# Performance work log

Measured on AMD Instinct MI355X. Metric: run time of the kernel, lower is better.

Reference implementation:

```python
import jax, jax.numpy as jnp
import numpy as np

N = 50000          # nodes
E = 600000         # edges
D = 128            # g_dim = h1_dim = h2_dim
R = 8              # 2 * n_speakers**2, n_speakers=2
B = 10             # num_bases


def setup_inputs() -> dict:
    key = jax.random.key(0)
    ks = jax.random.split(key, 10)
    s = 1.0 / np.sqrt(D)
    return {
        "node_features": jax.random.normal(ks[0], (N, D), jnp.float32),
        "edge_index": jax.random.randint(ks[1], (2, E), 0, N, jnp.int64),
        "edge_type": jax.random.randint(ks[2], (E,), 0, R, jnp.int64),
        # RGCNConv params (basis decomposition)
        "basis": jax.random.normal(ks[3], (B, D, D), jnp.float32) * s,
        "comp": jax.random.normal(ks[4], (R, B), jnp.float32) * (1.0 / np.sqrt(B)),
        "root": jax.random.normal(ks[5], (D, D), jnp.float32) * s,
        "bias1": jnp.zeros((D,), jnp.float32),
        # GraphConv params
        "w_rel": jax.random.normal(ks[6], (D, D), jnp.float32) * s,
        "b_rel": jnp.zeros((D,), jnp.float32),
        "w_root": jax.random.normal(ks[7], (D, D), jnp.float32) * s,
    }


def reference(node_features, edge_index, edge_type, basis, comp, root, bias1, w_rel, b_rel, w_root):
    x = node_features
    n = x.shape[0]
    r = comp.shape[0]
    src, dst = edge_index[0], edge_index[1]

    # ---- RGCNConv (basis decomposition, per-relation mean aggregation) ----
    # project through bases once: [N, B, D]
    xb = jnp.einsum('ni,bio->nbo', x, basis)
    # per-edge message: combine bases with relation coefficients  [E, D]
    msg = jnp.einsum('eb,ebo->eo', comp[edge_type], xb[src])
    # per-(dst, relation) mean normalization
    seg = dst * r + edge_type                       # [E]
    cnt = jax.ops.segment_sum(jnp.ones((msg.shape[0],), x.dtype), seg, num_segments=n * r)
    norm = 1.0 / jnp.maximum(cnt[seg], 1.0)         # [E]
    agg = jax.ops.segment_sum(msg * norm[:, None], dst, num_segments=n)  # [N, D]
    h1 = agg + x @ root + bias1

    # ---- GraphConv (add aggregation of neighbors + root transform) ----
    nbr = jax.ops.segment_sum(h1[src], dst, num_segments=n)  # [N, D]
    out = nbr @ w_rel.T + b_rel + h1 @ w_root.T
    return out
```

## Files before the change

### kernel.cpp

```cpp
#include <hip/hip_runtime.h>
#include <stdint.h>

#define N_NODES 50000
#define E_EDGES 600000
#define D 128
#define R_REL 8
#define B_BASES 10
#define RN (R_REL * N_NODES)
#define SCAN_B 1024

typedef __attribute__((ext_vector_type(8))) short bf16x8;
typedef __attribute__((ext_vector_type(4))) float f32x4;

__device__ __forceinline__ short f2b(float f) {
    uint32_t u = __float_as_uint(f);
    u += 0x7fff + ((u >> 16) & 1);
    return (short)(u >> 16);
}
__device__ __forceinline__ float b2f(uint16_t u) {
    return __uint_as_float((uint32_t)u << 16);
}

__global__ __launch_bounds__(256) void k_prep(const float* __restrict__ basis,
                                              const float* __restrict__ comp,
                                              const float* __restrict__ root,
                                              const float* __restrict__ wrel,
                                              const float* __restrict__ wroot,
                                              short* __restrict__ wt,
                                              short* __restrict__ root_t,
                                              short* __restrict__ wrel_b,
                                              short* __restrict__ wroot_b) {
    int tid = blockIdx.x * 256 + threadIdx.x;
    if (tid < R_REL * D * D) {
        int r = tid >> 14;
        int rem = tid & 16383;
        int j = rem >> 7, i = rem & 127;
        float s = 0.f;
#pragma unroll
        for (int b = 0; b < B_BASES; b++)
            s += comp[r * B_BASES + b] * basis[b * D * D + i * D + j];
        wt[tid] = f2b(s);
    } else {
        int t2 = tid - R_REL * D * D;
        if (t2 < D * D) {
            int j = t2 >> 7, i = t2 & 127;
            root_t[t2]  = f2b(root[i * D + j]);
            wrel_b[t2]  = f2b(wrel[t2]);
            wroot_b[t2] = f2b(wroot[t2]);
        }
    }
}

__global__ __launch_bounds__(256) void k_x2b(const float* __restrict__ x,
                                             unsigned short* __restrict__ xb) {
    int tid = blockIdx.x * 256 + threadIdx.x;
    if (tid >= N_NODES * D / 8) return;
    const float4* s = (const float4*)x + (size_t)tid * 2;
    float4 v0 = s[0], v1 = s[1];
    union { uint4 u; unsigned short h[8]; } pk;
    pk.h[0] = (unsigned short)f2b(v0.x); pk.h[1] = (unsigned short)f2b(v0.y);
    pk.h[2] = (unsigned short)f2b(v0.z); pk.h[3] = (unsigned short)f2b(v0.w);
    pk.h[4] = (unsigned short)f2b(v1.x); pk.h[5] = (unsigned short)f2b(v1.y);
    pk.h[6] = (unsigned short)f2b(v1.z); pk.h[7] = (unsigned short)f2b(v1.w);
    ((uint4*)xb)[tid] = pk.u;
}

__global__ __launch_bounds__(256) void k_count(const int* __restrict__ dst,
                                               const int* __restrict__ et,
                                               int* __restrict__ cntr) {
    int e = blockIdx.x * 256 + threadIdx.x;
    if (e >= E_EDGES) return;
    atomicAdd(&cntr[dst[e] * R_REL + et[e]], 1);
}

__global__ __launch_bounds__(SCAN_B) void k_scan_a(const int* __restrict__ in,
                                                   int* __restrict__ out,
                                                   int* __restrict__ bsum, int n) {
    __shared__ int lds[SCAN_B];
    int t = threadIdx.x, g = blockIdx.x * SCAN_B + t;
    int v = (g < n) ? in[g] : 0;
    lds[t] = v;
    __syncthreads();
    for (int off = 1; off < SCAN_B; off <<= 1) {
        int tv = (t >= off) ? lds[t - off] : 0;
        __syncthreads();
        lds[t] += tv;
        __syncthreads();
    }
    if (g < n) out[g] = lds[t] - v;
    if (t == SCAN_B - 1) bsum[blockIdx.x] = lds[t];
}

__global__ __launch_bounds__(SCAN_B) void k_scan_b(int* __restrict__ bsum, int nb) {
    __shared__ int lds[SCAN_B];
    int t = threadIdx.x;
    int v = (t < nb) ? bsum[t] : 0;
    lds[t] = v;
    __syncthreads();
    for (int off = 1; off < SCAN_B; off <<= 1) {
        int tv = (t >= off) ? lds[t - off] : 0;
        __syncthreads();
        lds[t] += tv;
        __syncthreads();
    }
    if (t < nb) bsum[t] = lds[t] - v;
}

__global__ __launch_bounds__(SCAN_B) void k_scan_c(int* __restrict__ out,
                                                   const int* __restrict__ bsum, int n) {
    int g = blockIdx.x * SCAN_B + threadIdx.x;
    if (g < n) out[g] += bsum[blockIdx.x];
}

__global__ __launch_bounds__(256) void k_bucket(const int* __restrict__ src,
                                                const int* __restrict__ dst,
                                                const int* __restrict__ et,
                                                const int* __restrict__ seg_off,
                                                int* __restrict__ cur,
                                                int* __restrict__ es1) {
    int e = blockIdx.x * 256 + threadIdx.x;
    if (e >= E_EDGES) return;
    int key = dst[e] * R_REL + et[e];
    int pos = seg_off[key] + atomicAdd(&cur[key], 1);
    es1[pos] = src[e];
}

__global__ __launch_bounds__(256) void k_ygemm(const unsigned short* __restrict__ xb,
                                               const short* __restrict__ wt, int r0,
                                               unsigned short* __restrict__ ybig) {
    __shared__ short xs[64 * 128];
    __shared__ short ws[128 * 128];
    int slice = blockIdx.y;
    const short* w = wt + (size_t)(r0 + slice) * D * D;
    unsigned short* y = ybig + (size_t)slice * N_NODES * D;
    int base = blockIdx.x * 64;
    int t = threadIdx.x;
    const uint4* wsrc = (const uint4*)w;
    for (int idx = t; idx < 2048; idx += 256) {
        int j = idx >> 4, c = idx & 15;
        *(uint4*)&ws[j * 128 + ((c ^ (j & 15)) << 3)] = wsrc[idx];
    }
    for (int idx = t; idx < 1024; idx += 256) {
        int row = idx >> 4, c = idx & 15;
        int node = base + row;
        uint4 v = make_uint4(0, 0, 0, 0);
        if (node < N_NODES) v = ((const uint4*)(xb + (size_t)node * D))[c];
        *(uint4*)&xs[row * 128 + ((c ^ (row & 15)) << 3)] = v;
    }
    __syncthreads();

    int wave = t >> 6, lane = t & 63, quad = lane >> 4, l16 = lane & 15;
    f32x4 acc[8];
#pragma unroll
    for (int jt = 0; jt < 8; jt++) acc[jt] = (f32x4){0.f, 0.f, 0.f, 0.f};
#pragma unroll
    for (int kc = 0; kc < 4; kc++) {
        int c0 = kc * 4 + quad;
        bf16x8 a = *(const bf16x8*)&xs[(wave * 16 + l16) * 128 + ((c0 ^ l16) << 3)];
#pragma unroll
        for (int jt = 0; jt < 8; jt++) {
            bf16x8 b = *(const bf16x8*)&ws[(jt * 16 + l16) * 128 + ((c0 ^ l16) << 3)];
            acc[jt] = __builtin_amdgcn_mfma_f32_16x16x32_bf16(a, b, acc[jt], 0, 0, 0);
        }
    }
#pragma unroll
    for (int reg = 0; reg < 4; reg++) {
        int node = base + wave * 16 + quad * 4 + reg;
        if (node >= N_NODES) continue;
#pragma unroll
        for (int jt = 0; jt < 8; jt++)
            y[(size_t)node * D + jt * 16 + l16] = (unsigned short)f2b(acc[jt][reg]);
    }
}

__global__ __launch_bounds__(256) void k_gemm_root(const unsigned short* __restrict__ inb,
                                                   const short* __restrict__ bt,
                                                   const float* __restrict__ bias,
                                                   const float* __restrict__ prev,
                                                   unsigned short* __restrict__ outb) {
    __shared__ short xs[64 * 128];
    __shared__ short ws[128 * 128];
    int base = blockIdx.x * 64;
    int t = threadIdx.x;
    const uint4* wsrc = (const uint4*)bt;
    for (int idx = t; idx < 2048; idx += 256) {
        int j = idx >> 4, c = idx & 15;
        *(uint4*)&ws[j * 128 + ((c ^ (j & 15)) << 3)] = wsrc[idx];
    }
    for (int idx = t; idx < 1024; idx += 256) {
        int row = idx >> 4, c = idx & 15;
        int node = base + row;
        uint4 v = make_uint4(0, 0, 0, 0);
        if (node < N_NODES) v = ((const uint4*)(inb + (size_t)node * D))[c];
        *(uint4*)&xs[row * 128 + ((c ^ (row & 15)) << 3)] = v;
    }
    __syncthreads();

    int wave = t >> 6, lane = t & 63, quad = lane >> 4, l16 = lane & 15;
    f32x4 acc[8];
#pragma unroll
    for (int jt = 0; jt < 8; jt++) acc[jt] = (f32x4){0.f, 0.f, 0.f, 0.f};
#pragma unroll
    for (int kc = 0; kc < 4; kc++) {
        int c0 = kc * 4 + quad;
        bf16x8 a = *(const bf16x8*)&xs[(wave * 16 + l16) * 128 + ((c0 ^ l16) << 3)];
#pragma unroll
        for (int jt = 0; jt < 8; jt++) {
            bf16x8 b = *(const bf16x8*)&ws[(jt * 16 + l16) * 128 + ((c0 ^ l16) << 3)];
            acc[jt] = __builtin_amdgcn_mfma_f32_16x16x32_bf16(a, b, acc[jt], 0, 0, 0);
        }
    }
#pragma unroll
    for (int reg = 0; reg < 4; reg++) {
        int node = base + wave * 16 + quad * 4 + reg;
        if (node >= N_NODES) continue;
#pragma unroll
        for (int jt = 0; jt < 8; jt++) {
            int col = jt * 16 + l16;
            float v = acc[jt][reg] + bias[col] + prev[(size_t)node * D + col];
            outb[(size_t)node * D + col] = (unsigned short)f2b(v);
        }
    }
}

__global__ __launch_bounds__(256) void k_agg4(const unsigned short* __restrict__ y,
                                              const int* __restrict__ es1,
                                              const int* __restrict__ cntr,
                                              const int* __restrict__ seg_off,
                                              float* __restrict__ h1, int phase) {
    int t = threadIdx.x;
    int wave = t >> 6, lane = t & 63, sub = lane >> 4, l = lane & 15;
    int d = blockIdx.x * 16 + wave * 4 + sub;
    if (d >= N_NODES) return;
    int kb = d * R_REL + phase * 4;
    int b0 = seg_off[kb], b1 = seg_off[kb + 1], b2 = seg_off[kb + 2], b3 = seg_off[kb + 3];
    int c3 = cntr[kb + 3];
    int end = b3 + c3;
    int c0 = b1 - b0, c1 = b2 - b1, c2 = b3 - b2;
    float n0 = c0 ? 1.f / (float)c0 : 0.f;
    float n1 = c1 ? 1.f / (float)c1 : 0.f;
    float n2 = c2 ? 1.f / (float)c2 : 0.f;
    float n3 = c3 ? 1.f / (float)c3 : 0.f;

    float acc[8];
#pragma unroll
    for (int j = 0; j < 8; j++) acc[j] = 0.f;
    size_t loff = (size_t)l * 8;

    int pos = b0;
    for (; pos + 4 <= end; pos += 4) {
        int i0 = es1[pos], i1 = es1[pos + 1], i2 = es1[pos + 2], i3 = es1[pos + 3];
        float m0 = (pos     >= b1) ? ((pos     >= b3) ? n3 : (pos     >= b2) ? n2 : n1) : n0;
        float m1 = (pos + 1 >= b1) ? ((pos + 1 >= b3) ? n3 : (pos + 1 >= b2) ? n2 : n1) : n0;
        float m2 = (pos + 2 >= b1) ? ((pos + 2 >= b3) ? n3 : (pos + 2 >= b2) ? n2 : n1) : n0;
        float m3 = (pos + 3 >= b1) ? ((pos + 3 >= b3) ? n3 : (pos + 3 >= b2) ? n2 : n1) : n0;
        int r0 = (pos     >= b1) + (pos     >= b2) + (pos     >= b3);
        int r1 = (pos + 1 >= b1) + (pos + 1 >= b2) + (pos + 1 >= b3);
        int r2 = (pos + 2 >= b1) + (pos + 2 >= b2) + (pos + 2 >= b3);
        int r3 = (pos + 3 >= b1) + (pos + 3 >= b2) + (pos + 3 >= b3);
        uint4 v0 = *(const uint4*)(y + ((size_t)r0 * N_NODES + i0) * D + loff);
        uint4 v1 = *(const uint4*)(y + ((size_t)r1 * N_NODES + i1) * D + loff);
        uint4 v2 = *(const uint4*)(y + ((size_t)r2 * N_NODES + i2) * D + loff);
        uint4 v3 = *(const uint4*)(y + ((size_t)r3 * N_NODES + i3) * D + loff);
        const uint32_t* w0 = (const uint32_t*)&v0;
        const uint32_t* w1 = (const uint32_t*)&v1;
        const uint32_t* w2 = (const uint32_t*)&v2;
        const uint32_t* w3 = (const uint32_t*)&v3;
#pragma unroll
        for (int q = 0; q < 4; q++) {
            acc[q * 2]     += m0 * b2f((uint16_t)w0[q]) + m1 * b2f((uint16_t)w1[q]) +
                              m2 * b2f((uint16_t)w2[q]) + m3 * b2f((uint16_t)w3[q]);
            acc[q * 2 + 1] += m0 * b2f((uint16_t)(w0[q] >> 16)) + m1 * b2f((uint16_t)(w1[q] >> 16)) +
                              m2 * b2f((uint16_t)(w2[q] >> 16)) + m3 * b2f((uint16_t)(w3[q] >> 16));
        }
    }
    for (; pos < end; pos++) {
        int i0 = es1[pos];
        float m0 = (pos >= b1) ? ((pos >= b3) ? n3 : (pos >= b2) ? n2 : n1) : n0;
        int r0 = (pos >= b1) + (pos >= b2) + (pos >= b3);
        uint4 v0 = *(const uint4*)(y + ((size_t)r0 * N_NODES + i0) * D + loff);
        const uint32_t* w0 = (const uint32_t*)&v0;
#pragma unroll
        for (int q = 0; q < 4; q++) {
            acc[q * 2]     += m0 * b2f((uint16_t)w0[q]);
            acc[q * 2 + 1] += m0 * b2f((uint16_t)(w0[q] >> 16));
        }
    }

    float* hr = h1 + (size_t)d * D + loff;
    if (phase) {
#pragma unroll
        for (int j = 0; j < 8; j++) acc[j] += hr[j];
    }
    *(float4*)hr = make_float4(acc[0], acc[1], acc[2], acc[3]);
    *(float4*)(hr + 4) = make_float4(acc[4], acc[5], acc[6], acc[7]);
}

__global__ __launch_bounds__(256) void k_agg_nbr(const unsigned short* __restrict__ h1b,
                                                 const int* __restrict__ es1,
                                                 const int* __restrict__ seg_off,
                                                 unsigned short* __restrict__ nbr) {
    int t = threadIdx.x;
    int wave = t >> 6, lane = t & 63, sub = lane >> 4, l = lane & 15;
    int d = blockIdx.x * 16 + wave * 4 + sub;
    if (d >= N_NODES) return;
    int s0 = seg_off[d * R_REL];
    int end = (d == N_NODES - 1) ? E_EDGES : seg_off[(d + 1) * R_REL];
    float acc[8];
#pragma unroll
    for (int j = 0; j < 8; j++) acc[j] = 0.f;
    size_t loff = (size_t)l * 8;

    int pos = s0;
    for (; pos + 4 <= end; pos += 4) {
        int i0 = es1[pos], i1 = es1[pos + 1], i2 = es1[pos + 2], i3 = es1[pos + 3];
        uint4 v0 = *(const uint4*)(h1b + (size_t)i0 * D + loff);
        uint4 v1 = *(const uint4*)(h1b + (size_t)i1 * D + loff);
        uint4 v2 = *(const uint4*)(h1b + (size_t)i2 * D + loff);
        uint4 v3 = *(const uint4*)(h1b + (size_t)i3 * D + loff);
        const uint32_t* w0 = (const uint32_t*)&v0;
        const uint32_t* w1 = (const uint32_t*)&v1;
        const uint32_t* w2 = (const uint32_t*)&v2;
        const uint32_t* w3 = (const uint32_t*)&v3;
#pragma unroll
        for (int q = 0; q < 4; q++) {
            acc[q * 2]     += b2f((uint16_t)w0[q]) + b2f((uint16_t)w1[q]) +
                              b2f((uint16_t)w2[q]) + b2f((uint16_t)w3[q]);
            acc[q * 2 + 1] += b2f((uint16_t)(w0[q] >> 16)) + b2f((uint16_t)(w1[q] >> 16)) +
                              b2f((uint16_t)(w2[q] >> 16)) + b2f((uint16_t)(w3[q] >> 16));
        }
    }
    for (; pos < end; pos++) {
        int i0 = es1[pos];
        uint4 v0 = *(const uint4*)(h1b + (size_t)i0 * D + loff);
        const uint32_t* w0 = (const uint32_t*)&v0;
#pragma unroll
        for (int q = 0; q < 4; q++) {
            acc[q * 2]     += b2f((uint16_t)w0[q]);
            acc[q * 2 + 1] += b2f((uint16_t)(w0[q] >> 16));
        }
    }

    union { uint4 u; unsigned short h[8]; } pk;
#pragma unroll
    for (int j = 0; j < 8; j++) pk.h[j] = (unsigned short)f2b(acc[j]);
    *(uint4*)(nbr + (size_t)d * D + loff) = pk.u;
}

__global__ __launch_bounds__(256) void k_out2(const unsigned short* __restrict__ h1b,
                                              const unsigned short* __restrict__ nbr,
                                              const short* __restrict__ wroot_b,
                                              const short* __restrict__ wrel_b,
                                              const float* __restrict__ brel,
                                              float* __restrict__ out) {
    __shared__ short xs1[64 * 128];
    __shared__ short xs2[64 * 128];
    __shared__ short ws1[128 * 128];
    __shared__ short ws2[128 * 128];
    int base = blockIdx.x * 64;
    int t = threadIdx.x;
    const uint4* w1 = (const uint4*)wroot_b;
    const uint4* w2 = (const uint4*)wrel_b;
    for (int idx = t; idx < 2048; idx += 256) {
        int j = idx >> 4, c = idx & 15;
        int sw = j * 128 + ((c ^ (j & 15)) << 3);
        *(uint4*)&ws1[sw] = w1[idx];
        *(uint4*)&ws2[sw] = w2[idx];
    }
    for (int idx = t; idx < 1024; idx += 256) {
        int row = idx >> 4, c = idx & 15;
        int node = base + row;
        uint4 v1 = make_uint4(0, 0, 0, 0), v2 = make_uint4(0, 0, 0, 0);
        if (node < N_NODES) {
            v1 = ((const uint4*)(h1b + (size_t)node * D))[c];
            v2 = ((const uint4*)(nbr + (size_t)node * D))[c];
        }
        int sw = row * 128 + ((c ^ (row & 15)) << 3);
        *(uint4*)&xs1[sw] = v1;
        *(uint4*)&xs2[sw] = v2;
    }
    __syncthreads();

    int wave = t >> 6, lane = t & 63, quad = lane >> 4, l16 = lane & 15;
    f32x4 acc[8];
#pragma unroll
    for (int jt = 0; jt < 8; jt++) acc[jt] = (f32x4){0.f, 0.f, 0.f, 0.f};
#pragma unroll
    for (int kc = 0; kc < 4; kc++) {
        int c0 = kc * 4 + quad;
        int arow = (wave * 16 + l16) * 128 + ((c0 ^ l16) << 3);
        bf16x8 a1 = *(const bf16x8*)&xs1[arow];
        bf16x8 a2 = *(const bf16x8*)&xs2[arow];
#pragma unroll
        for (int jt = 0; jt < 8; jt++) {
            int brow = (jt * 16 + l16) * 128 + ((c0 ^ l16) << 3);
            bf16x8 b1 = *(const bf16x8*)&ws1[brow];
            bf16x8 b2 = *(const bf16x8*)&ws2[brow];
            acc[jt] = __builtin_amdgcn_mfma_f32_16x16x32_bf16(a1, b1, acc[jt], 0, 0, 0);
            acc[jt] = __builtin_amdgcn_mfma_f32_16x16x32_bf16(a2, b2, acc[jt], 0, 0, 0);
        }
    }
#pragma unroll
    for (int reg = 0; reg < 4; reg++) {
        int node = base + wave * 16 + quad * 4 + reg;
        if (node >= N_NODES) continue;
#pragma unroll
        for (int jt = 0; jt < 8; jt++) {
            int col = jt * 16 + l16;
            out[(size_t)node * D + col] = acc[jt][reg] + brel[col];
        }
    }
}

extern "C" void kernel_launch(void* const* d_in, const int* in_sizes, int n_in,
                              void* d_out, int out_size, void* d_ws, size_t ws_size,
                              hipStream_t stream) {
    const float* x     = (const float*)d_in[0];
    const int*   ei    = (const int*)d_in[1];
    const int*   et    = (const int*)d_in[2];
    const float* basis = (const float*)d_in[3];
    const float* comp  = (const float*)d_in[4];
    const float* root  = (const float*)d_in[5];
    const float* bias1 = (const float*)d_in[6];
    const float* wrel  = (const float*)d_in[7];
    const float* brel  = (const float*)d_in[8];
    const float* wroot = (const float*)d_in[9];
    float* out = (float*)d_out;
    const int* src = ei;
    const int* dst = ei + E_EDGES;

    char* p = (char*)d_ws;
    auto alloc = [&](size_t bytes) { char* q = p; p += (bytes + 255) & ~(size_t)255; return q; };
    short* wt      = (short*)alloc((size_t)R_REL * D * D * sizeof(short));
    short* root_t  = (short*)alloc(D * D * sizeof(short));
    short* wrel_b  = (short*)alloc(D * D * sizeof(short));
    short* wroot_b = (short*)alloc(D * D * sizeof(short));
    int*   cntr    = (int*)alloc((size_t)2 * RN * sizeof(int));
    int*   cur     = cntr + RN;
    int*   seg_off = (int*)alloc((size_t)RN * sizeof(int));
    int*   es1     = (int*)alloc((size_t)(E_EDGES + 16) * sizeof(int));
    int*   bsum    = (int*)alloc(SCAN_B * sizeof(int));
    unsigned short* xb   = (unsigned short*)alloc((size_t)N_NODES * D * sizeof(unsigned short));
    unsigned short* ybig = (unsigned short*)alloc((size_t)4 * N_NODES * D * sizeof(unsigned short));
    float* h1      = (float*)alloc((size_t)N_NODES * D * sizeof(float));
    unsigned short* h1b  = (unsigned short*)alloc((size_t)N_NODES * D * sizeof(unsigned short));
    unsigned short* nbr  = xb;

    hipMemsetAsync(cntr, 0, (size_t)2 * RN * sizeof(int), stream);

    k_prep<<<(R_REL * D * D + D * D + 255) / 256, 256, 0, stream>>>(
        basis, comp, root, wrel, wroot, wt, root_t, wrel_b, wroot_b);
    k_x2b<<<(N_NODES * D / 8 + 255) / 256, 256, 0, stream>>>(x, xb);
    k_count<<<(E_EDGES + 255) / 256, 256, 0, stream>>>(dst, et, cntr);

    int nscan = (RN + SCAN_B - 1) / SCAN_B;
    k_scan_a<<<nscan, SCAN_B, 0, stream>>>(cntr, seg_off, bsum, RN);
    k_scan_b<<<1, SCAN_B, 0, stream>>>(bsum, nscan);
    k_scan_c<<<nscan, SCAN_B, 0, stream>>>(seg_off, bsum, RN);

    k_bucket<<<(E_EDGES + 255) / 256, 256, 0, stream>>>(src, dst, et, seg_off, cur, es1);

    int nb = (N_NODES + 63) / 64;
    int na = (N_NODES + 15) / 16;

    k_ygemm<<<dim3(nb, 4), 256, 0, stream>>>(xb, wt, 0, ybig);
    k_agg4<<<na, 256, 0, stream>>>(ybig, es1, cntr, seg_off, h1, 0);
    k_ygemm<<<dim3(nb, 4), 256, 0, stream>>>(xb, wt, 4, ybig);
    k_agg4<<<na, 256, 0, stream>>>(ybig, es1, cntr, seg_off, h1, 1);

    k_gemm_root<<<nb, 256, 0, stream>>>(xb, root_t, bias1, h1, h1b);
    k_agg_nbr<<<na, 256, 0, stream>>>(h1b, es1, seg_off, nbr);
    k_out2<<<nb, 256, 0, stream>>>(h1b, nbr, wroot_b, wrel_b, brel, out);
}
```

Measured before the change: 325.5 us.

## Merge relation GEMMs with root GEMM, single-pass aggregation, wave-shuffle scan

Folds the root transform in as a ninth weight slice, so one batched GEMM writes all nine projections and a single aggregation kernel produces h1 in bf16 without an fp32 intermediate or a second pass. The bucket step now increments seg_off in place, so seg_off ends up holding segment end offsets. It packs the relation into each edge index and precomputes per-edge norms, removing per-position branch logic. Smaller launches are merged (cast and count fused, scan uses wave shuffles, the scan-b kernel is reused), and the cur counter array is dropped. The trade-off is a larger ybig buffer (9 slices instead of 4) and an extra per-edge norm array to read.

```diff
diff --git a/kernel.cpp b/kernel.cpp
--- a/kernel.cpp
+++ b/kernel.cpp
@@ -7,7 +7,6 @@
 #define R_REL 8
 #define B_BASES 10
 #define RN (R_REL * N_NODES)
-#define SCAN_B 1024
 
 typedef __attribute__((ext_vector_type(8))) short bf16x8;
 typedef __attribute__((ext_vector_type(4))) float f32x4;
@@ -27,111 +26,113 @@
                                               const float* __restrict__ wrel,
                                               const float* __restrict__ wroot,
                                               short* __restrict__ wt,
-                                              short* __restrict__ root_t,
                                               short* __restrict__ wrel_b,
                                               short* __restrict__ wroot_b) {
     int tid = blockIdx.x * 256 + threadIdx.x;
-    if (tid < R_REL * D * D) {
-        int r = tid >> 14;
+    if (tid < 9 * D * D) {
+        int s = tid >> 14;
         int rem = tid & 16383;
         int j = rem >> 7, i = rem & 127;
-        float s = 0.f;
-#pragma unroll
-        for (int b = 0; b < B_BASES; b++)
-            s += comp[r * B_BASES + b] * basis[b * D * D + i * D + j];
-        wt[tid] = f2b(s);
+        float v;
+        if (s < 8) {
+            v = 0.f;
+#pragma unroll
+            for (int b = 0; b < B_BASES; b++)
+                v += comp[s * B_BASES + b] * basis[b * D * D + i * D + j];
+        } else {
+            v = root[i * D + j];
+        }
+        wt[tid] = f2b(v);
     } else {
-        int t2 = tid - R_REL * D * D;
+        int t2 = tid - 9 * D * D;
         if (t2 < D * D) {
-            int j = t2 >> 7, i = t2 & 127;
-            root_t[t2]  = f2b(root[i * D + j]);
             wrel_b[t2]  = f2b(wrel[t2]);
             wroot_b[t2] = f2b(wroot[t2]);
         }
     }
 }
 
-__global__ __launch_bounds__(256) void k_x2b(const float* __restrict__ x,
-                                             unsigned short* __restrict__ xb) {
+__global__ __launch_bounds__(256) void k_misc(const float* __restrict__ x,
+                                              unsigned short* __restrict__ xb,
+                                              const int* __restrict__ dst,
+                                              const int* __restrict__ et,
+                                              int* __restrict__ cntr) {
     int tid = blockIdx.x * 256 + threadIdx.x;
-    if (tid >= N_NODES * D / 8) return;
-    const float4* s = (const float4*)x + (size_t)tid * 2;
-    float4 v0 = s[0], v1 = s[1];
-    union { uint4 u; unsigned short h[8]; } pk;
-    pk.h[0] = (unsigned short)f2b(v0.x); pk.h[1] = (unsigned short)f2b(v0.y);
-    pk.h[2] = (unsigned short)f2b(v0.z); pk.h[3] = (unsigned short)f2b(v0.w);
-    pk.h[4] = (unsigned short)f2b(v1.x); pk.h[5] = (unsigned short)f2b(v1.y);
-    pk.h[6] = (unsigned short)f2b(v1.z); pk.h[7] = (unsigned short)f2b(v1.w);
-    ((uint4*)xb)[tid] = pk.u;
-}
-
-__global__ __launch_bounds__(256) void k_count(const int* __restrict__ dst,
-                                               const int* __restrict__ et,
-                                               int* __restrict__ cntr) {
-    int e = blockIdx.x * 256 + threadIdx.x;
-    if (e >= E_EDGES) return;
-    atomicAdd(&cntr[dst[e] * R_REL + et[e]], 1);
-}
-
-__global__ __launch_bounds__(SCAN_B) void k_scan_a(const int* __restrict__ in,
-                                                   int* __restrict__ out,
-                                                   int* __restrict__ bsum, int n) {
-    __shared__ int lds[SCAN_B];
-    int t = threadIdx.x, g = blockIdx.x * SCAN_B + t;
+    if (tid < N_NODES * D / 8) {
+        const float4* s = (const float4*)x + (size_t)tid * 2;
+        float4 v0 = s[0], v1 = s[1];
+        union { uint4 u; unsigned short h[8]; } pk;
+        pk.h[0] = (unsigned short)f2b(v0.x); pk.h[1] = (unsigned short)f2b(v0.y);
+        pk.h[2] = (unsigned short)f2b(v0.z); pk.h[3] = (unsigned short)f2b(v0.w);
+        pk.h[4] = (unsigned short)f2b(v1.x); pk.h[5] = (unsigned short)f2b(v1.y);
+        pk.h[6] = (unsigned short)f2b(v1.z); pk.h[7] = (unsigned short)f2b(v1.w);
+        ((uint4*)xb)[tid] = pk.u;
+    } else {
+        int e = tid - N_NODES * D / 8;
+        if (e < E_EDGES)
+            atomicAdd(&cntr[dst[e] * R_REL + et[e]], 1);
+    }
+}
+
+__device__ __forceinline__ int wave_scan_incl(int v) {
+    int lane = threadIdx.x & 63;
+#pragma unroll
+    for (int off = 1; off < 64; off <<= 1) {
+        int n = __shfl_up(v, off, 64);
+        if (lane >= off) v += n;
+    }
+    return v;
+}
+
+__global__ __launch_bounds__(1024) void k_scan_a(const int* __restrict__ in,
+                                                 int* __restrict__ out,
+                                                 int* __restrict__ bsum, int n) {
+    __shared__ int wsum[16];
+    int t = threadIdx.x, lane = t & 63, wid = t >> 6;
+    int g = blockIdx.x * 1024 + t;
     int v = (g < n) ? in[g] : 0;
-    lds[t] = v;
+    int isc = wave_scan_incl(v);
+    if (lane == 63) wsum[wid] = isc;
     __syncthreads();
-    for (int off = 1; off < SCAN_B; off <<= 1) {
-        int tv = (t >= off) ? lds[t - off] : 0;
-        __syncthreads();
-        lds[t] += tv;
-        __syncthreads();
-    }
-    if (g < n) out[g] = lds[t] - v;
-    if (t == SCAN_B - 1) bsum[blockIdx.x] = lds[t];
-}
-
-__global__ __launch_bounds__(SCAN_B) void k_scan_b(int* __restrict__ bsum, int nb) {
-    __shared__ int lds[SCAN_B];
-    int t = threadIdx.x;
-    int v = (t < nb) ? bsum[t] : 0;
-    lds[t] = v;
+    if (wid == 0) {
+        int wv = (lane < 16) ? wsum[lane] : 0;
+        int wsc = wave_scan_incl(wv);
+        if (lane < 16) wsum[lane] = wsc - wv;
+    }
     __syncthreads();
-    for (int off = 1; off < SCAN_B; off <<= 1) {
-        int tv = (t >= off) ? lds[t - off] : 0;
-        __syncthreads();
-        lds[t] += tv;
-        __syncthreads();
-    }
-    if (t < nb) bsum[t] = lds[t] - v;
-}
-
-__global__ __launch_bounds__(SCAN_B) void k_scan_c(int* __restrict__ out,
-                                                   const int* __restrict__ bsum, int n) {
-    int g = blockIdx.x * SCAN_B + threadIdx.x;
+    if (g < n) out[g] = wsum[wid] + isc - v;
+    if (t == 1023 && bsum) bsum[blockIdx.x] = wsum[15] + isc;
+}
+
+__global__ __launch_bounds__(1024) void k_scan_c(int* __restrict__ out,
+                                                 const int* __restrict__ bsum, int n) {
+    int g = blockIdx.x * 1024 + threadIdx.x;
     if (g < n) out[g] += bsum[blockIdx.x];
 }
 
 __global__ __launch_bounds__(256) void k_bucket(const int* __restrict__ src,
                                                 const int* __restrict__ dst,
                                                 const int* __restrict__ et,
-                                                const int* __restrict__ seg_off,
-                                                int* __restrict__ cur,
-                                                int* __restrict__ es1) {
+                                                const int* __restrict__ cntr,
+                                                int* __restrict__ seg_off,
+                                                int* __restrict__ es1,
+                                                float* __restrict__ enorm) {
     int e = blockIdx.x * 256 + threadIdx.x;
     if (e >= E_EDGES) return;
-    int key = dst[e] * R_REL + et[e];
-    int pos = seg_off[key] + atomicAdd(&cur[key], 1);
-    es1[pos] = src[e];
+    int r = et[e];
+    int key = dst[e] * R_REL + r;
+    int pos = atomicAdd(&seg_off[key], 1);
+    es1[pos] = (src[e] << 3) | r;
+    enorm[pos] = 1.0f / (float)cntr[key];
 }
 
 __global__ __launch_bounds__(256) void k_ygemm(const unsigned short* __restrict__ xb,
-                                               const short* __restrict__ wt, int r0,
+                                               const short* __restrict__ wt,
                                                unsigned short* __restrict__ ybig) {
     __shared__ short xs[64 * 128];
     __shared__ short ws[128 * 128];
     int slice = blockIdx.y;
-    const short* w = wt + (size_t)(r0 + slice) * D * D;
+    const short* w = wt + (size_t)slice * D * D;
     unsigned short* y = ybig + (size_t)slice * N_NODES * D;
     int base = blockIdx.x * 64;
     int t = threadIdx.x;
@@ -173,95 +174,31 @@
     }
 }
 
-__global__ __launch_bounds__(256) void k_gemm_root(const unsigned short* __restrict__ inb,
-                                                   const short* __restrict__ bt,
-                                                   const float* __restrict__ bias,
-                                                   const float* __restrict__ prev,
-                                                   unsigned short* __restrict__ outb) {
-    __shared__ short xs[64 * 128];
-    __shared__ short ws[128 * 128];
-    int base = blockIdx.x * 64;
-    int t = threadIdx.x;
-    const uint4* wsrc = (const uint4*)bt;
-    for (int idx = t; idx < 2048; idx += 256) {
-        int j = idx >> 4, c = idx & 15;
-        *(uint4*)&ws[j * 128 + ((c ^ (j & 15)) << 3)] = wsrc[idx];
-    }
-    for (int idx = t; idx < 1024; idx += 256) {
-        int row = idx >> 4, c = idx & 15;
-        int node = base + row;
-        uint4 v = make_uint4(0, 0, 0, 0);
-        if (node < N_NODES) v = ((const uint4*)(inb + (size_t)node * D))[c];
-        *(uint4*)&xs[row * 128 + ((c ^ (row & 15)) << 3)] = v;
-    }
-    __syncthreads();
-
-    int wave = t >> 6, lane = t & 63, quad = lane >> 4, l16 = lane & 15;
-    f32x4 acc[8];
-#pragma unroll
-    for (int jt = 0; jt < 8; jt++) acc[jt] = (f32x4){0.f, 0.f, 0.f, 0.f};
-#pragma unroll
-    for (int kc = 0; kc < 4; kc++) {
-        int c0 = kc * 4 + quad;
-        bf16x8 a = *(const bf16x8*)&xs[(wave * 16 + l16) * 128 + ((c0 ^ l16) << 3)];
-#pragma unroll
-        for (int jt = 0; jt < 8; jt++) {
-            bf16x8 b = *(const bf16x8*)&ws[(jt * 16 + l16) * 128 + ((c0 ^ l16) << 3)];
-            acc[jt] = __builtin_amdgcn_mfma_f32_16x16x32_bf16(a, b, acc[jt], 0, 0, 0);
-        }
-    }
-#pragma unroll
-    for (int reg = 0; reg < 4; reg++) {
-        int node = base + wave * 16 + quad * 4 + reg;
-        if (node >= N_NODES) continue;
-#pragma unroll
-        for (int jt = 0; jt < 8; jt++) {
-            int col = jt * 16 + l16;
-            float v = acc[jt][reg] + bias[col] + prev[(size_t)node * D + col];
-            outb[(size_t)node * D + col] = (unsigned short)f2b(v);
-        }
-    }
-}
-
-__global__ __launch_bounds__(256) void k_agg4(const unsigned short* __restrict__ y,
+__global__ __launch_bounds__(256) void k_agg8(const unsigned short* __restrict__ ybig,
                                               const int* __restrict__ es1,
-                                              const int* __restrict__ cntr,
+                                              const float* __restrict__ enorm,
                                               const int* __restrict__ seg_off,
-                                              float* __restrict__ h1, int phase) {
+                                              const float* __restrict__ bias1,
+                                              unsigned short* __restrict__ h1b) {
     int t = threadIdx.x;
     int wave = t >> 6, lane = t & 63, sub = lane >> 4, l = lane & 15;
     int d = blockIdx.x * 16 + wave * 4 + sub;
     if (d >= N_NODES) return;
-    int kb = d * R_REL + phase * 4;
-    int b0 = seg_off[kb], b1 = seg_off[kb + 1], b2 = seg_off[kb + 2], b3 = seg_off[kb + 3];
-    int c3 = cntr[kb + 3];
-    int end = b3 + c3;
-    int c0 = b1 - b0, c1 = b2 - b1, c2 = b3 - b2;
-    float n0 = c0 ? 1.f / (float)c0 : 0.f;
-    float n1 = c1 ? 1.f / (float)c1 : 0.f;
-    float n2 = c2 ? 1.f / (float)c2 : 0.f;
-    float n3 = c3 ? 1.f / (float)c3 : 0.f;
-
+    int start = (d == 0) ? 0 : seg_off[d * R_REL - 1];
+    int end = seg_off[d * R_REL + 7];
     float acc[8];
 #pragma unroll
     for (int j = 0; j < 8; j++) acc[j] = 0.f;
     size_t loff = (size_t)l * 8;
 
-    int pos = b0;
+    int pos = start;
     for (; pos + 4 <= end; pos += 4) {
-        int i0 = es1[pos], i1 = es1[pos + 1], i2 = es1[pos + 2], i3 = es1[pos + 3];
-        float m0 = (pos     >= b1) ? ((pos     >= b3) ? n3 : (pos     >= b2) ? n2 : n1) : n0;
-        float m1 = (pos + 1 >= b1) ? ((pos + 1 >= b3) ? n3 : (pos + 1 >= b2) ? n2 : n1) : n0;
-        float m2 = (pos + 2 >= b1) ? ((pos + 2 >= b3) ? n3 : (pos + 2 >= b2) ? n2 : n1) : n0;
-        float m3 = (pos + 3 >= b1) ? ((pos + 3 >= b3) ? n3 : (pos + 3 >= b2) ? n2 : n1) : n0;
-        int r0 = (pos     >= b1) + (pos     >= b2) + (pos     >= b3);
-        int r1 = (pos + 1 >= b1) + (pos + 1 >= b2) + (pos + 1 >= b3);
-        int r2 = (pos + 2 >= b1) + (pos + 2 >= b2) + (pos + 2 >= b3);
-        int r3 = (pos + 3 >= b1) + (pos + 3 >= b2) + (pos + 3 >= b3);
-        uint4 v0 = *(const uint4*)(y + ((size_t)r0 * N_NODES + i0) * D + loff);
-        uint4 v1 = *(const uint4*)(y + ((size_t)r1 * N_NODES + i1) * D + loff);
-        uint4 v2 = *(const uint4*)(y + ((size_t)r2 * N_NODES + i2) * D + loff);
-        uint4 v3 = *(const uint4*)(y + ((size_t)r3 * N_NODES + i3) * D + loff);
+        int p0 = es1[pos], p1 = es1[pos + 1], p2 = es1[pos + 2], p3 = es1[pos + 3];
+        float m0 = enorm[pos], m1 = enorm[pos + 1], m2 = enorm[pos + 2], m3 = enorm[pos + 3];
+        uint4 v0 = *(const uint4*)(ybig + ((size_t)(p0 & 7) * N_NODES + (p0 >> 3)) * D + loff);
+        uint4 v1 = *(const uint4*)(ybig + ((size_t)(p1 & 7) * N_NODES + (p1 >> 3)) * D + loff);
+        uint4 v2 = *(const uint4*)(ybig + ((size_t)(p2 & 7) * N_NODES + (p2 >> 3)) * D + loff);
+        uint4 v3 = *(const uint4*)(ybig + ((size_t)(p3 & 7) * N_NODES + (p3 >> 3)) * D + loff);
         const uint32_t* w0 = (const uint32_t*)&v0;
         const uint32_t* w1 = (const uint32_t*)&v1;
         const uint32_t* w2 = (const uint32_t*)&v2;
@@ -275,10 +212,9 @@
         }
     }
     for (; pos < end; pos++) {
-        int i0 = es1[pos];
-        float m0 = (pos >= b1) ? ((pos >= b3) ? n3 : (pos >= b2) ? n2 : n1) : n0;
-        int r0 = (pos >= b1) + (pos >= b2) + (pos >= b3);
-        uint4 v0 = *(const uint4*)(y + ((size_t)r0 * N_NODES + i0) * D + loff);
+        int p0 = es1[pos];
+        float m0 = enorm[pos];
+        uint4 v0 = *(const uint4*)(ybig + ((size_t)(p0 & 7) * N_NODES + (p0 >> 3)) * D + loff);
         const uint32_t* w0 = (const uint32_t*)&v0;
 #pragma unroll
         for (int q = 0; q < 4; q++) {
@@ -287,13 +223,18 @@
         }
     }
 
-    float* hr = h1 + (size_t)d * D + loff;
-    if (phase) {
-#pragma unroll
-        for (int j = 0; j < 8; j++) acc[j] += hr[j];
-    }
-    *(float4*)hr = make_float4(acc[0], acc[1], acc[2], acc[3]);
-    *(float4*)(hr + 4) = make_float4(acc[4], acc[5], acc[6], acc[7]);
+    uint4 rv = *(const uint4*)(ybig + ((size_t)8 * N_NODES + d) * D + loff);
+    const uint32_t* rw = (const uint32_t*)&rv;
+    float4 ba = *(const float4*)(bias1 + l * 8);
+    float4 bb = *(const float4*)(bias1 + l * 8 + 4);
+    float bv[8] = {ba.x, ba.y, ba.z, ba.w, bb.x, bb.y, bb.z, bb.w};
+    union { uint4 u; unsigned short h[8]; } pk;
+#pragma unroll
+    for (int q = 0; q < 4; q++) {
+        pk.h[q * 2]     = (unsigned short)f2b(acc[q * 2] + b2f((uint16_t)rw[q]) + bv[q * 2]);
+        pk.h[q * 2 + 1] = (unsigned short)f2b(acc[q * 2 + 1] + b2f((uint16_t)(rw[q] >> 16)) + bv[q * 2 + 1]);
+    }
+    *(uint4*)(h1b + (size_t)d * D + loff) = pk.u;
 }
 
 __global__ __launch_bounds__(256) void k_agg_nbr(const unsigned short* __restrict__ h1b,
@@ -304,16 +245,17 @@
     int wave = t >> 6, lane = t & 63, sub = lane >> 4, l = lane & 15;
     int d = blockIdx.x * 16 + wave * 4 + sub;
     if (d >= N_NODES) return;
-    int s0 = seg_off[d * R_REL];
-    int end = (d == N_NODES - 1) ? E_EDGES : seg_off[(d + 1) * R_REL];
+    int start = (d == 0) ? 0 : seg_off[d * R_REL - 1];
+    int end = seg_off[d * R_REL + 7];
     float acc[8];
 #pragma unroll
     for (int j = 0; j < 8; j++) acc[j] = 0.f;
     size_t loff = (size_t)l * 8;
 
-    int pos = s0;
+    int pos = start;
     for (; pos + 4 <= end; pos += 4) {
-        int i0 = es1[pos], i1 = es1[pos + 1], i2 = es1[pos + 2], i3 = es1[pos + 3];
+        int i0 = es1[pos] >> 3, i1 = es1[pos + 1] >> 3;
+        int i2 = es1[pos + 2] >> 3, i3 = es1[pos + 3] >> 3;
         uint4 v0 = *(const uint4*)(h1b + (size_t)i0 * D + loff);
         uint4 v1 = *(const uint4*)(h1b + (size_t)i1 * D + loff);
         uint4 v2 = *(const uint4*)(h1b + (size_t)i2 * D + loff);
@@ -331,7 +273,7 @@
         }
     }
     for (; pos < end; pos++) {
-        int i0 = es1[pos];
+        int i0 = es1[pos] >> 3;
         uint4 v0 = *(const uint4*)(h1b + (size_t)i0 * D + loff);
         const uint32_t* w0 = (const uint32_t*)&v0;
 #pragma unroll
@@ -431,44 +373,37 @@
 
     char* p = (char*)d_ws;
     auto alloc = [&](size_t bytes) { char* q = p; p += (bytes + 255) & ~(size_t)255; return q; };
-    short* wt      = (short*)alloc((size_t)R_REL * D * D * sizeof(short));
-    short* root_t  = (short*)alloc(D * D * sizeof(short));
+    short* wt      = (short*)alloc((size_t)9 * D * D * sizeof(short));
     short* wrel_b  = (short*)alloc(D * D * sizeof(short));
     short* wroot_b = (short*)alloc(D * D * sizeof(short));
-    int*   cntr    = (int*)alloc((size_t)2 * RN * sizeof(int));
-    int*   cur     = cntr + RN;
+    int*   cntr    = (int*)alloc((size_t)RN * sizeof(int));
     int*   seg_off = (int*)alloc((size_t)RN * sizeof(int));
     int*   es1     = (int*)alloc((size_t)(E_EDGES + 16) * sizeof(int));
-    int*   bsum    = (int*)alloc(SCAN_B * sizeof(int));
+    float* enorm   = (float*)alloc((size_t)(E_EDGES + 16) * sizeof(float));
+    int*   bsum    = (int*)alloc(1024 * sizeof(int));
     unsigned short* xb   = (unsigned short*)alloc((size_t)N_NODES * D * sizeof(unsigned short));
-    unsigned short* ybig = (unsigned short*)alloc((size_t)4 * N_NODES * D * sizeof(unsigned short));
-    float* h1      = (float*)alloc((size_t)N_NODES * D * sizeof(float));
+    unsigned short* ybig = (unsigned short*)alloc((size_t)9 * N_NODES * D * sizeof(unsigned short));
     unsigned short* h1b  = (unsigned short*)alloc((size_t)N_NODES * D * sizeof(unsigned short));
     unsigned short* nbr  = xb;
 
-    hipMemsetAsync(cntr, 0, (size_t)2 * RN * sizeof(int), stream);
-
-    k_prep<<<(R_REL * D * D + D * D + 255) / 256, 256, 0, stream>>>(
-        basis, comp, root, wrel, wroot, wt, root_t, wrel_b, wroot_b);
-    k_x2b<<<(N_NODES * D / 8 + 255) / 256, 256, 0, stream>>>(x, xb);
-    k_count<<<(E_EDGES + 255) / 256, 256, 0, stream>>>(dst, et, cntr);
-
-    int nscan = (RN + SCAN_B - 1) / SCAN_B;
-    k_scan_a<<<nscan, SCAN_B, 0, stream>>>(cntr, seg_off, bsum, RN);
-    k_scan_b<<<1, SCAN_B, 0, stream>>>(bsum, nscan);
-    k_scan_c<<<nscan, SCAN_B, 0, stream>>>(seg_off, bsum, RN);
-
-    k_bucket<<<(E_EDGES + 255) / 256, 256, 0, stream>>>(src, dst, et, seg_off, cur, es1);
+    hipMemsetAsync(cntr, 0, (size_t)RN * sizeof(int), stream);
+
+    k_prep<<<(9 * D * D + D * D + 255) / 256, 256, 0, stream>>>(
+        basis, comp, root, wrel, wroot, wt, wrel_b, wroot_b);
+    k_misc<<<(N_NODES * D / 8 + E_EDGES + 255) / 256, 256, 0, stream>>>(x, xb, dst, et, cntr);
+
+    int nscan = (RN + 1023) / 1024;
+    k_scan_a<<<nscan, 1024, 0, stream>>>(cntr, seg_off, bsum, RN);
+    k_scan_a<<<1, 1024, 0, stream>>>(bsum, bsum, nullptr, nscan);
+    k_scan_c<<<nscan, 1024, 0, stream>>>(seg_off, bsum, RN);
+
+    k_bucket<<<(E_EDGES + 255) / 256, 256, 0, stream>>>(src, dst, et, cntr, seg_off, es1, enorm);
 
     int nb = (N_NODES + 63) / 64;
     int na = (N_NODES + 15) / 16;
 
-    k_ygemm<<<dim3(nb, 4), 256, 0, stream>>>(xb, wt, 0, ybig);
-    k_agg4<<<na, 256, 0, stream>>>(ybig, es1, cntr, seg_off, h1, 0);
-    k_ygemm<<<dim3(nb, 4), 256, 0, stream>>>(xb, wt, 4, ybig);
-    k_agg4<<<na, 256, 0, stream>>>(ybig, es1, cntr, seg_off, h1, 1);
-
-    k_gemm_root<<<nb, 256, 0, stream>>>(xb, root_t, bias1, h1, h1b);
+    k_ygemm<<<dim3(nb, 9), 256, 0, stream>>>(xb, wt, ybig);
+    k_agg8<<<na, 256, 0, stream>>>(ybig, es1, enorm, seg_off, bias1, h1b);
     k_agg_nbr<<<na, 256, 0, stream>>>(h1b, es1, seg_off, nbr);
     k_out2<<<nb, 256, 0, stream>>>(h1b, nbr, wroot_b, wrel_b, brel, out);
 }
```

Result: faster. 287.4 us (-11.7%).
